# Optimization experiments

Hardware: AMD Instinct MI355X
Metric: run time of the kernel (lower is better)

The kernel has to match this reference:

```python
import jax, jax.numpy as jnp
import numpy as np
from jax import lax

D, B, C, H, HD, FF, NC = 6, 32, 384, 6, 64, 1536, 10
IMG, P = 224, 16
N = (IMG // P) ** 2 + 1  # 197 tokens incl cls
SCALE = HD ** -0.5
EPS = 1e-6


def ln(x, w, b):
    m = jnp.mean(x, axis=-1, keepdims=True)
    v = jnp.var(x, axis=-1, keepdims=True)
    return (x - m) * lax.rsqrt(v + EPS) * w + b


def setup_inputs() -> dict:
    key = jax.random.key(0)
    ks = iter(jax.random.split(key, 40))
    rn = lambda shape, s=0.02: jax.random.normal(next(ks), shape, jnp.float32) * s
    inp = {
        'x': jax.random.normal(next(ks), (B, 3, IMG, IMG), jnp.float32),
        'y': jax.random.randint(next(ks), (B,), 0, NC),
        'patch_w': rn((C, 3, P, P)),
        'patch_b': rn((C,)),
        'cls_token': rn((1, 1, C)),
        'pos_embed': rn((1, N, C)),
        'n1_w': jnp.ones((D, C)), 'n1_b': jnp.zeros((D, C)),
        'qkv_w': rn((D, 3 * C, C)), 'qkv_b': rn((D, 3 * C)),
        'proj_w': rn((D, C, C)), 'proj_b': rn((D, C)),
        'mask_attn': jnp.ones((D, NC, H, HD)) + rn((D, NC, H, HD), 0.01),
        'mask_proj': jnp.ones((D, NC, C, C)) + rn((D, NC, C, C), 0.01),
        'n2_w': jnp.ones((D, C)), 'n2_b': jnp.zeros((D, C)),
        'fc1_w': rn((D, FF, C)), 'fc1_b': rn((D, FF)),
        'fc2_w': rn((D, C, FF)), 'fc2_b': rn((D, C)),
        'mask_fc1': jnp.ones((D, NC, FF, C)) + rn((D, NC, FF, C), 0.01),
        'mask_fc2': jnp.ones((D, NC, C, FF)) + rn((D, NC, C, FF), 0.01),
        'norm_w': jnp.ones((C,)), 'norm_b': jnp.zeros((C,)),
        'head_w': rn((NC, C)), 'head_b': jnp.zeros((NC,)),
    }
    return inp


def reference(x, y, patch_w, patch_b, cls_token, pos_embed, n1_w, n1_b, qkv_w,
              qkv_b, proj_w, proj_b, mask_attn, mask_proj, n2_w, n2_b,
              fc1_w, fc1_b, fc2_w, fc2_b, mask_fc1, mask_fc2,
              norm_w, norm_b, head_w, head_b):
    # patch embed: conv P x P stride P -> (B, C, 14, 14) -> (B, 196, C)
    h = lax.conv_general_dilated(x, patch_w, (P, P), 'VALID',
                                 dimension_numbers=('NCHW', 'OIHW', 'NCHW'))
    h = h.reshape(B, C, -1).transpose(0, 2, 1) + patch_b
    h = jnp.concatenate([jnp.broadcast_to(cls_token, (B, 1, C)), h], axis=1)
    h = h + pos_embed

    def block(xc, p):
        (w1n, b1n, qw, qb, pw, pb, ma, mp, w2n, b2n,
         f1w, f1b, f2w, f2b, mf1, mf2) = p
        t = ln(xc, w1n, b1n)
        qkv = (t @ qw.T + qb).reshape(B, N, 3, H, HD).transpose(2, 0, 3, 1, 4)
        q, k, v = qkv[0], qkv[1], qkv[2]  # (B,H,N,HD)
        a = jax.nn.softmax((q * SCALE) @ k.transpose(0, 1, 3, 2), axis=-1)
        o = a @ v  # (B,H,N,HD)
        o = o * ma[y][:, :, None, :]  # per-class head/dim mask
        o = o.transpose(0, 2, 1, 3).reshape(B, N, C)
        Wp = pw[None] * mp[y]  # (B,C,C) per-sample masked proj
        attn_out = jnp.einsum('bni,boi->bno', o, Wp) + pb
        xc = xc + attn_out
        t = ln(xc, w2n, b2n)
        W1 = f1w[None] * mf1[y]  # (B,FF,C)
        t = jnp.einsum('bni,boi->bno', t, W1) + f1b
        t = jax.nn.gelu(t, approximate=False)
        W2 = f2w[None] * mf2[y]  # (B,C,FF)
        t = jnp.einsum('bni,boi->bno', t, W2) + f2b
        return xc + t, None

    xs = (n1_w, n1_b, qkv_w, qkv_b, proj_w, proj_b, mask_attn, mask_proj,
          n2_w, n2_b, fc1_w, fc1_b, fc2_w, fc2_b, mask_fc1, mask_fc2)
    h, _ = lax.scan(block, h, xs)
    h = ln(h, norm_w, norm_b)
    cls = h[:, 0]  # (B, C)
    return cls @ head_w.T + head_b
```

## Files before the change

### kernel.cpp

```cpp
#include <hip/hip_runtime.h>
#include <hip/hip_bf16.h>
#include <math.h>

#define Dn 6
#define Bn 32
#define Cn 384
#define Hn 6
#define HDn 64
#define FFn 1536
#define NCn 10
#define IMGn 224
#define Nn 197
#define NPATCH 196
#define RP 256
#define SCALEf 0.125f
#define EPSf 1e-6f

typedef unsigned short u16;
typedef __attribute__((ext_vector_type(8))) short short8;
typedef __attribute__((ext_vector_type(4))) float f32x4;

__device__ __forceinline__ u16 f2bf(float f) {
    unsigned u = __float_as_uint(f);
    return (u16)((u + 0x7FFFu + ((u >> 16) & 1u)) >> 16);
}

__device__ __forceinline__ void gload16(const void* g, void* l) {
    __builtin_amdgcn_global_load_lds((const __attribute__((address_space(1))) void*)g,
                                     (__attribute__((address_space(3))) void*)l, 16, 0, 0);
}

__global__ __launch_bounds__(256) void cvtbf_kernel(const float* __restrict__ in,
                                                    u16* __restrict__ out) {
    long off = ((long)blockIdx.x * 256 + threadIdx.x) * 8;
    float4 v0 = *(const float4*)(in + off);
    float4 v1 = *(const float4*)(in + off + 4);
    short8 p;
    p[0] = f2bf(v0.x); p[1] = f2bf(v0.y); p[2] = f2bf(v0.z); p[3] = f2bf(v0.w);
    p[4] = f2bf(v1.x); p[5] = f2bf(v1.y); p[6] = f2bf(v1.z); p[7] = f2bf(v1.w);
    *(short8*)(out + off) = p;
}

__global__ __launch_bounds__(256) void maskmul3_kernel(
    const float* __restrict__ pw, const float* __restrict__ mp,
    const float* __restrict__ f1w, const float* __restrict__ mf1,
    const float* __restrict__ f2w, const float* __restrict__ mf2,
    u16* __restrict__ WMp, u16* __restrict__ WMf1, u16* __restrict__ WMf2) {
    int seg = blockIdx.y;
    const float* W; const float* M; u16* O; int NK; int nblk;
    if (seg == 0)      { W = pw;  M = mp;  O = WMp;  NK = Cn * Cn;  nblk = 720; }
    else if (seg == 1) { W = f1w; M = mf1; O = WMf1; NK = FFn * Cn; nblk = 2880; }
    else               { W = f2w; M = mf2; O = WMf2; NK = Cn * FFn; nblk = 2880; }
    if (blockIdx.x >= nblk) return;
    long e = ((long)blockIdx.x * 256 + threadIdx.x) * 8;
    int c = (int)(e / NK);
    int wi = (int)(e - (long)c * NK);
    float4 w0 = *(const float4*)(W + wi);
    float4 w1 = *(const float4*)(W + wi + 4);
    float4 m0 = *(const float4*)(M + e);
    float4 m1 = *(const float4*)(M + e + 4);
    short8 p;
    p[0] = f2bf(w0.x * m0.x); p[1] = f2bf(w0.y * m0.y);
    p[2] = f2bf(w0.z * m0.z); p[3] = f2bf(w0.w * m0.w);
    p[4] = f2bf(w1.x * m1.x); p[5] = f2bf(w1.y * m1.y);
    p[6] = f2bf(w1.z * m1.z); p[7] = f2bf(w1.w * m1.w);
    *(short8*)(O + e) = p;
}

__global__ __launch_bounds__(256) void im2col_kernel(const float* __restrict__ x,
                                                     u16* __restrict__ col) {
    long idx = (long)blockIdx.x * 256 + threadIdx.x;
    int k = (int)(idx % 768);
    long row = idx / 768;
    int b = (int)(row / NPATCH), p = (int)(row % NPATCH);
    int i = k / 256, r = k % 256, ph = r / 16, pw = r % 16;
    int py = p / 14, px = p % 14;
    col[idx] = f2bf(x[(((long)b * 3 + i) * IMGn + py * 16 + ph) * IMGn + px * 16 + pw]);
}

__global__ __launch_bounds__(256) void assemble_kernel(const float* __restrict__ tmp,
                                                       const float* __restrict__ cls_token,
                                                       const float* __restrict__ pos,
                                                       float* __restrict__ x) {
    long idx = (long)blockIdx.x * 256 + threadIdx.x;
    const long total = (long)Bn * Nn * Cn;
    if (idx >= total) return;
    int c = (int)(idx % Cn);
    long rem = idx / Cn;
    int n = (int)(rem % Nn);
    int b = (int)(rem / Nn);
    float v;
    if (n == 0) v = cls_token[c];
    else v = tmp[((long)b * NPATCH + (n - 1)) * Cn + c];
    x[((long)b * RP + n) * Cn + c] = v + pos[n * Cn + c];
}

__global__ __launch_bounds__(64) void ln_kernel(const float* __restrict__ x,
                                                const float* __restrict__ w,
                                                const float* __restrict__ b,
                                                u16* __restrict__ out) {
    long blk = blockIdx.x;
    int bb = (int)(blk / Nn), n = (int)(blk % Nn);
    long row = (long)bb * RP + n;
    int lane = threadIdx.x;
    const float* xr = x + row * Cn;
    float v[6];
    float s = 0.f, ss = 0.f;
#pragma unroll
    for (int j = 0; j < 6; ++j) {
        v[j] = xr[lane + 64 * j];
        s += v[j];
        ss += v[j] * v[j];
    }
#pragma unroll
    for (int off = 32; off >= 1; off >>= 1) {
        s += __shfl_xor(s, off);
        ss += __shfl_xor(ss, off);
    }
    float m = s * (1.0f / Cn);
    float var = ss * (1.0f / Cn) - m * m;
    float rstd = rsqrtf(var + EPSf);
#pragma unroll
    for (int j = 0; j < 6; ++j) {
        int c = lane + 64 * j;
        out[row * Cn + c] = f2bf((v[j] - m) * rstd * w[c] + b[c]);
    }
}

template <int EPI, int MT>
__global__ __launch_bounds__(256) void gemm_bf16(
    const u16* __restrict__ A, long strideA,
    const u16* __restrict__ Wb, long wClassStride,
    const int* __restrict__ y,
    const float* __restrict__ bias,
    void* __restrict__ OutV, long strideO,
    int Nout, int Ktot) {
    const int bz = blockIdx.z;
    A += (long)bz * strideA;
    const u16* Wp = Wb + (y ? (long)y[bz] * wClassStride : 0);

    constexpr int ASUB = MT / 16;
    constexpr int AI = MT / 32;
    __shared__ alignas(16) u16 Ab[2][ASUB * 512];
    __shared__ alignas(16) u16 Bb[2][4096];

    const int tid = threadIdx.x;
    const int lane = tid & 63;
    const int w = tid >> 6;
    const int wr = w >> 1, wc = w & 1;
    const int m0 = blockIdx.x * MT;
    const int n0 = blockIdx.y * 128;
    const int r15 = lane & 15, oct = lane >> 4;

    auto STAGE = [&](int k0, int bf) {
        {
            int s0 = 2 * w;
            const u16* b0 = Wp + (long)(n0 + 16 * s0 + r15) * Ktot + k0 + oct * 8;
            gload16(b0, &Bb[bf][s0 * 512]);
            gload16(b0 + 16 * (long)Ktot, &Bb[bf][(s0 + 1) * 512]);
        }
        if (MT == 128) {
            int s0 = 2 * w;
            const u16* a0 = A + (long)(m0 + 16 * s0 + r15) * Ktot + k0 + oct * 8;
            gload16(a0, &Ab[bf][s0 * 512]);
            gload16(a0 + 16 * (long)Ktot, &Ab[bf][(s0 + 1) * 512]);
        } else {
            const u16* a0 = A + (long)(m0 + 16 * w + r15) * Ktot + k0 + oct * 8;
            gload16(a0, &Ab[bf][w * 512]);
        }
    };

    f32x4 acc[AI][4];
#pragma unroll
    for (int i = 0; i < AI; ++i)
#pragma unroll
        for (int j = 0; j < 4; ++j) acc[i][j] = (f32x4){0.f, 0.f, 0.f, 0.f};

    const int nsteps = Ktot / 32;
    STAGE(0, 0);
    __syncthreads();
    int cur = 0;
    for (int t = 0; t < nsteps; ++t) {
        if (t + 1 < nsteps) STAGE((t + 1) * 32, cur ^ 1);
        short8 af[AI], bfr[4];
#pragma unroll
        for (int i = 0; i < AI; ++i)
            af[i] = *(const short8*)(&Ab[cur][(wr * AI + i) * 512 + lane * 8]);
#pragma unroll
        for (int j = 0; j < 4; ++j)
            bfr[j] = *(const short8*)(&Bb[cur][(wc * 4 + j) * 512 + lane * 8]);
#pragma unroll
        for (int i = 0; i < AI; ++i)
#pragma unroll
            for (int j = 0; j < 4; ++j)
                acc[i][j] = __builtin_amdgcn_mfma_f32_16x16x32_bf16(af[i], bfr[j], acc[i][j], 0, 0, 0);
        __syncthreads();
        cur ^= 1;
    }

    const int lr = lane >> 4;
    const int lc = lane & 15;
#pragma unroll
    for (int i = 0; i < AI; ++i) {
#pragma unroll
        for (int j = 0; j < 4; ++j) {
            int colg = n0 + (wc * 4 + j) * 16 + lc;
            float bv = bias ? bias[colg] : 0.f;
#pragma unroll
            for (int r = 0; r < 4; ++r) {
                int m = m0 + (wr * AI + i) * 16 + lr * 4 + r;
                float v = acc[i][j][r] + bv;
                long oi = (long)m * Nout + colg;
                if (EPI == 0) {
                    ((u16*)OutV + (long)bz * strideO)[oi] = f2bf(v);
                } else if (EPI == 1) {
                    v = 0.5f * v * (1.0f + erff(v * 0.70710678118654752440f));
                    ((u16*)OutV + (long)bz * strideO)[oi] = f2bf(v);
                } else if (EPI == 2) {
                    float* Out = (float*)OutV + (long)bz * strideO;
                    Out[oi] += v;
                } else {
                    ((float*)OutV + (long)bz * strideO)[oi] = v;
                }
            }
        }
    }
}

__global__ __launch_bounds__(256) void attn_fused(const u16* __restrict__ qkv,
                                                  const float* __restrict__ ma,
                                                  const int* __restrict__ y,
                                                  u16* __restrict__ O) {
    const int it = blockIdx.x;
    const int bh = blockIdx.y;
    const int h = bh % Hn, b = bh / Hn;
    const int i0 = it * 64;
    const int tid = threadIdx.x, lane = tid & 63, w = tid >> 6;
    const int lg = lane >> 4, lc = lane & 15;

    __shared__ alignas(16) u16 SH[31744];
    u16* Qb = SH;
    u16* Kb = SH + 4096;
    u16* Vb = SH;
    u16* Pb = SH + 17408;

    const u16* qkv_b = qkv + (long)b * RP * (3 * Cn);
    const int r15 = lane & 15;
    const int oct = lane >> 4;

#pragma unroll
    for (int si = 0; si < 2; ++si) {
        int s = w * 2 + si;
        int r = (s >> 1) * 16 + r15;
        int g = (s & 1) * 4 + oct;
        const u16* src = qkv_b + (long)(i0 + r) * (3 * Cn) + h * HDn + g * 8;
        gload16(src, Qb + s * 512);
    }
    for (int s = w; s < 26; s += 4) {
        int c = (s >> 1) * 16 + r15;
        int g = (s & 1) * 4 + oct;
        const u16* src = qkv_b + (long)c * (3 * Cn) + Cn + h * HDn + g * 8;
        gload16(src, Kb + s * 512);
    }
    __syncthreads();

    f32x4 s[13];
#pragma unroll
    for (int jf = 0; jf < 13; ++jf) s[jf] = (f32x4){0.f, 0.f, 0.f, 0.f};
    {
        short8 a0 = *(const short8*)(Qb + (w * 2 + 0) * 512 + lane * 8);
        short8 a1 = *(const short8*)(Qb + (w * 2 + 1) * 512 + lane * 8);
#pragma unroll
        for (int jf = 0; jf < 13; ++jf) {
            short8 b0 = *(const short8*)(Kb + (jf * 2 + 0) * 512 + lane * 8);
            short8 b1 = *(const short8*)(Kb + (jf * 2 + 1) * 512 + lane * 8);
            s[jf] = __builtin_amdgcn_mfma_f32_16x16x32_bf16(a0, b0, s[jf], 0, 0, 0);
            s[jf] = __builtin_amdgcn_mfma_f32_16x16x32_bf16(a1, b1, s[jf], 0, 0, 0);
        }
    }

#pragma unroll
    for (int r = 0; r < 4; ++r) {
        float mx = -1e30f;
#pragma unroll
        for (int jf = 0; jf < 13; ++jf) {
            float v = s[jf][r] * SCALEf;
            if (jf * 16 + lc > 196) v = -1e30f;
            mx = fmaxf(mx, v);
        }
#pragma unroll
        for (int off = 1; off <= 8; off <<= 1) mx = fmaxf(mx, __shfl_xor(mx, off));
        float sum = 0.f;
#pragma unroll
        for (int jf = 0; jf < 13; ++jf) {
            float e = (jf * 16 + lc <= 196) ? __expf(s[jf][r] * SCALEf - mx) : 0.f;
            s[jf][r] = e;
            sum += e;
        }
#pragma unroll
        for (int off = 1; off <= 8; off <<= 1) sum += __shfl_xor(sum, off);
        float inv = 1.0f / sum;
#pragma unroll
        for (int jf = 0; jf < 13; ++jf) s[jf][r] *= inv;
    }
    __syncthreads();

    if (lane < 32) {
        short8 z = {0, 0, 0, 0, 0, 0, 0, 0};
        *(short8*)(Pb + (w * 7 + 6) * 512 + (32 + lane) * 8) = z;
    }
#pragma unroll
    for (int jf = 0; jf < 13; ++jf) {
#pragma unroll
        for (int r = 0; r < 4; ++r) {
            int col = jf * 16 + lc;
            int row = lg * 4 + r;
            Pb[(w * 7 + (col >> 5)) * 512 + (((col >> 3) & 3) * 16 + row) * 8 + (col & 7)] =
                (u16)f2bf(s[jf][r]);
        }
    }
    {
        const u16* vbase = qkv_b + 2 * Cn + h * HDn + (tid & 63);
        int d = tid & 63;
#pragma unroll
        for (int k = 0; k < 7; ++k) {
            int jo = (tid >> 6) + 4 * k;
            short8 p;
#pragma unroll
            for (int t = 0; t < 8; ++t)
                p[t] = (short)vbase[(long)(jo * 8 + t) * (3 * Cn)];
            *(short8*)(Vb + (d >> 4) * (7 * 512) + (jo >> 2) * 512 +
                       ((jo & 3) * 16 + (d & 15)) * 8) = p;
        }
    }
    __syncthreads();

    f32x4 o[4];
#pragma unroll
    for (int df = 0; df < 4; ++df) o[df] = (f32x4){0.f, 0.f, 0.f, 0.f};
#pragma unroll
    for (int ks = 0; ks < 7; ++ks) {
        short8 pa = *(const short8*)(Pb + (w * 7 + ks) * 512 + lane * 8);
#pragma unroll
        for (int df = 0; df < 4; ++df) {
            short8 vb = *(const short8*)(Vb + (df * 7 + ks) * 512 + lane * 8);
            o[df] = __builtin_amdgcn_mfma_f32_16x16x32_bf16(pa, vb, o[df], 0, 0, 0);
        }
    }

    const float* mar = ma + (long)y[b] * (Hn * HDn) + h * HDn;
#pragma unroll
    for (int df = 0; df < 4; ++df) {
        int dcol = df * 16 + lc;
        float mk = mar[dcol];
#pragma unroll
        for (int r = 0; r < 4; ++r) {
            int i = i0 + w * 16 + lg * 4 + r;
            O[((long)b * RP + i) * Cn + h * HDn + dcol] = f2bf(o[df][r] * mk);
        }
    }
}

__global__ __launch_bounds__(64) void final_head(const float* __restrict__ x,
                                                 const float* __restrict__ nw,
                                                 const float* __restrict__ nb,
                                                 const float* __restrict__ hw,
                                                 const float* __restrict__ hb,
                                                 float* __restrict__ out) {
    int b = blockIdx.x;
    int lane = threadIdx.x;
    const float* xr = x + (long)b * RP * Cn;
    float v[6];
    float s = 0.f, ss = 0.f;
#pragma unroll
    for (int j = 0; j < 6; ++j) {
        v[j] = xr[lane + 64 * j];
        s += v[j];
        ss += v[j] * v[j];
    }
#pragma unroll
    for (int off = 32; off >= 1; off >>= 1) {
        s += __shfl_xor(s, off);
        ss += __shfl_xor(ss, off);
    }
    float m = s * (1.0f / Cn);
    float var = ss * (1.0f / Cn) - m * m;
    float rstd = rsqrtf(var + EPSf);
    float nvals[6];
#pragma unroll
    for (int j = 0; j < 6; ++j) {
        int c = lane + 64 * j;
        nvals[j] = (v[j] - m) * rstd * nw[c] + nb[c];
    }
    for (int c10 = 0; c10 < NCn; ++c10) {
        float p = 0.f;
#pragma unroll
        for (int j = 0; j < 6; ++j) p += nvals[j] * hw[(long)c10 * Cn + lane + 64 * j];
#pragma unroll
        for (int off = 32; off >= 1; off >>= 1) p += __shfl_xor(p, off);
        if (lane == 0) out[b * NCn + c10] = p + hb[c10];
    }
}

extern "C" void kernel_launch(void* const* d_in, const int* in_sizes, int n_in,
                              void* d_out, int out_size, void* d_ws, size_t ws_size,
                              hipStream_t stream) {
    const float* x_in     = (const float*)d_in[0];
    const int*   y        = (const int*)d_in[1];
    const float* patch_w  = (const float*)d_in[2];
    const float* patch_b  = (const float*)d_in[3];
    const float* cls_tok  = (const float*)d_in[4];
    const float* pos_emb  = (const float*)d_in[5];
    const float* n1_w     = (const float*)d_in[6];
    const float* n1_b     = (const float*)d_in[7];
    const float* qkv_w    = (const float*)d_in[8];
    const float* qkv_b    = (const float*)d_in[9];
    const float* proj_w   = (const float*)d_in[10];
    const float* proj_b   = (const float*)d_in[11];
    const float* mask_attn= (const float*)d_in[12];
    const float* mask_proj= (const float*)d_in[13];
    const float* n2_w     = (const float*)d_in[14];
    const float* n2_b     = (const float*)d_in[15];
    const float* fc1_w    = (const float*)d_in[16];
    const float* fc1_b    = (const float*)d_in[17];
    const float* fc2_w    = (const float*)d_in[18];
    const float* fc2_b    = (const float*)d_in[19];
    const float* mask_fc1 = (const float*)d_in[20];
    const float* mask_fc2 = (const float*)d_in[21];
    const float* norm_w   = (const float*)d_in[22];
    const float* norm_b   = (const float*)d_in[23];
    const float* head_w   = (const float*)d_in[24];
    const float* head_b   = (const float*)d_in[25];

    char* base = (char*)d_ws;
    float* X   = (float*)base;                       base += (long)Bn * RP * Cn * 4;
    u16*   T   = (u16*)base;                         base += (long)Bn * RP * Cn * 2;
    u16*   QKV = (u16*)base;                         base += (long)Bn * RP * 3 * Cn * 2;
    u16*   O   = (u16*)base;                         base += (long)Bn * RP * Cn * 2;
    u16*   FFb = (u16*)base;                         base += (long)Bn * RP * FFn * 2;
    u16*   COL = (u16*)base;                         base += (long)Bn * NPATCH * 768 * 2;
    u16*   WQ  = (u16*)base;                         base += (long)Dn * 3 * Cn * Cn * 2;
    u16*   WP  = (u16*)base;                         base += (long)Cn * 768 * 2;
    u16*   WMp = (u16*)base;                         base += (long)NCn * Cn * Cn * 2;
    u16*   WMf1= (u16*)base;                         base += (long)NCn * FFn * Cn * 2;
    u16*   WMf2= (u16*)base;                         base += (long)NCn * Cn * FFn * 2;
    float* PTMP= (float*)FFb;

    const long sX = (long)RP * Cn;
    const long sT = (long)RP * Cn;
    const long sF = (long)RP * FFn;

    cvtbf_kernel<<<1296, 256, 0, stream>>>(qkv_w, WQ);
    cvtbf_kernel<<<144, 256, 0, stream>>>(patch_w, WP);

    im2col_kernel<<<18816, 256, 0, stream>>>(x_in, COL);
    gemm_bf16<3, 64><<<dim3(98, 3, 1), 256, 0, stream>>>(
        COL, 0, WP, 0, nullptr, patch_b, PTMP, 0, Cn, 768);
    assemble_kernel<<<9456, 256, 0, stream>>>(PTMP, cls_tok, pos_emb, X);

    for (int l = 0; l < Dn; ++l) {
        maskmul3_kernel<<<dim3(2880, 3), 256, 0, stream>>>(
            proj_w + (long)l * Cn * Cn, mask_proj + (long)l * NCn * Cn * Cn,
            fc1_w + (long)l * FFn * Cn, mask_fc1 + (long)l * NCn * FFn * Cn,
            fc2_w + (long)l * Cn * FFn, mask_fc2 + (long)l * NCn * Cn * FFn,
            WMp, WMf1, WMf2);

        ln_kernel<<<Bn * Nn, 64, 0, stream>>>(X, n1_w + l * Cn, n1_b + l * Cn, T);
        gemm_bf16<0, 128><<<dim3(64, 9, 1), 256, 0, stream>>>(
            T, 0, WQ + (long)l * 3 * Cn * Cn, 0, nullptr, qkv_b + (long)l * 3 * Cn,
            QKV, 0, 3 * Cn, Cn);
        attn_fused<<<dim3(4, Bn * Hn), 256, 0, stream>>>(
            QKV, mask_attn + (long)l * NCn * Hn * HDn, y, O);
        gemm_bf16<2, 64><<<dim3(4, 3, Bn), 256, 0, stream>>>(
            O, sT, WMp, (long)Cn * Cn, y, proj_b + l * Cn, X, sX, Cn, Cn);
        ln_kernel<<<Bn * Nn, 64, 0, stream>>>(X, n2_w + l * Cn, n2_b + l * Cn, T);
        gemm_bf16<1, 128><<<dim3(2, 12, Bn), 256, 0, stream>>>(
            T, sT, WMf1, (long)FFn * Cn, y, fc1_b + (long)l * FFn, FFb, sF, FFn, Cn);
        gemm_bf16<2, 64><<<dim3(4, 3, Bn), 256, 0, stream>>>(
            FFb, sF, WMf2, (long)Cn * FFn, y, fc2_b + l * Cn, X, sX, Cn, FFn);
    }

    final_head<<<Bn, 64, 0, stream>>>(X, norm_w, norm_b, head_w, head_b, (float*)d_out);
}
```

Baseline: 1.023 ms.

## Fuse residual add and LayerNorm into full-row GEMM epilogues, batch mask prep

Adds a gemm_ln kernel that computes full 384-wide output rows per block, so the residual add and the following LayerNorm run in the GEMM epilogue. This removes the standalone ln_kernel launches and the extra passes over X. The patch-embed GEMM also folds in the pos-embed add and the first LN, and a small kernel handles the cls token and zeroes the pad rows. Mask-weight products for all layers are now built in one up-front launch instead of once per layer, at the cost of more workspace. The proj and fc2 GEMMs now launch only 4 row-tiles per sample (128 blocks) with 24 accumulators per wave, which may reduce occupancy and parallelism.

```diff
diff --git a/kernel.cpp b/kernel.cpp
--- a/kernel.cpp
+++ b/kernel.cpp
@@ -41,16 +41,24 @@
     *(short8*)(out + off) = p;
 }
 
-__global__ __launch_bounds__(256) void maskmul3_kernel(
+__global__ __launch_bounds__(256) void maskmul_all(
     const float* __restrict__ pw, const float* __restrict__ mp,
     const float* __restrict__ f1w, const float* __restrict__ mf1,
     const float* __restrict__ f2w, const float* __restrict__ mf2,
     u16* __restrict__ WMp, u16* __restrict__ WMf1, u16* __restrict__ WMf2) {
+    int l = blockIdx.z;
     int seg = blockIdx.y;
     const float* W; const float* M; u16* O; int NK; int nblk;
-    if (seg == 0)      { W = pw;  M = mp;  O = WMp;  NK = Cn * Cn;  nblk = 720; }
-    else if (seg == 1) { W = f1w; M = mf1; O = WMf1; NK = FFn * Cn; nblk = 2880; }
-    else               { W = f2w; M = mf2; O = WMf2; NK = Cn * FFn; nblk = 2880; }
+    if (seg == 0) {
+        W = pw + (long)l * Cn * Cn; M = mp + (long)l * NCn * Cn * Cn;
+        O = WMp + (long)l * NCn * Cn * Cn; NK = Cn * Cn; nblk = 720;
+    } else if (seg == 1) {
+        W = f1w + (long)l * FFn * Cn; M = mf1 + (long)l * NCn * FFn * Cn;
+        O = WMf1 + (long)l * NCn * FFn * Cn; NK = FFn * Cn; nblk = 2880;
+    } else {
+        W = f2w + (long)l * Cn * FFn; M = mf2 + (long)l * NCn * Cn * FFn;
+        O = WMf2 + (long)l * NCn * Cn * FFn; NK = Cn * FFn; nblk = 2880;
+    }
     if (blockIdx.x >= nblk) return;
     long e = ((long)blockIdx.x * 256 + threadIdx.x) * 8;
     int c = (int)(e / NK);
@@ -78,101 +86,85 @@
     col[idx] = f2bf(x[(((long)b * 3 + i) * IMGn + py * 16 + ph) * IMGn + px * 16 + pw]);
 }
 
-__global__ __launch_bounds__(256) void assemble_kernel(const float* __restrict__ tmp,
-                                                       const float* __restrict__ cls_token,
-                                                       const float* __restrict__ pos,
-                                                       float* __restrict__ x) {
-    long idx = (long)blockIdx.x * 256 + threadIdx.x;
-    const long total = (long)Bn * Nn * Cn;
-    if (idx >= total) return;
-    int c = (int)(idx % Cn);
-    long rem = idx / Cn;
-    int n = (int)(rem % Nn);
-    int b = (int)(rem / Nn);
-    float v;
-    if (n == 0) v = cls_token[c];
-    else v = tmp[((long)b * NPATCH + (n - 1)) * Cn + c];
-    x[((long)b * RP + n) * Cn + c] = v + pos[n * Cn + c];
-}
-
-__global__ __launch_bounds__(64) void ln_kernel(const float* __restrict__ x,
-                                                const float* __restrict__ w,
-                                                const float* __restrict__ b,
-                                                u16* __restrict__ out) {
-    long blk = blockIdx.x;
-    int bb = (int)(blk / Nn), n = (int)(blk % Nn);
-    long row = (long)bb * RP + n;
-    int lane = threadIdx.x;
-    const float* xr = x + row * Cn;
-    float v[6];
-    float s = 0.f, ss = 0.f;
-#pragma unroll
-    for (int j = 0; j < 6; ++j) {
-        v[j] = xr[lane + 64 * j];
-        s += v[j];
-        ss += v[j] * v[j];
-    }
-#pragma unroll
-    for (int off = 32; off >= 1; off >>= 1) {
-        s += __shfl_xor(s, off);
-        ss += __shfl_xor(ss, off);
-    }
-    float m = s * (1.0f / Cn);
-    float var = ss * (1.0f / Cn) - m * m;
-    float rstd = rsqrtf(var + EPSf);
-#pragma unroll
-    for (int j = 0; j < 6; ++j) {
-        int c = lane + 64 * j;
-        out[row * Cn + c] = f2bf((v[j] - m) * rstd * w[c] + b[c]);
-    }
-}
-
-template <int EPI, int MT>
+__global__ __launch_bounds__(256) void clspad_kernel(const float* __restrict__ cls,
+                                                     const float* __restrict__ pos,
+                                                     const float* __restrict__ nw,
+                                                     const float* __restrict__ nb,
+                                                     float* __restrict__ X,
+                                                     u16* __restrict__ T) {
+    int b = blockIdx.x;
+    int tid = threadIdx.x;
+    float* Xb = X + (long)b * RP * Cn;
+    u16* Tb = T + (long)b * RP * Cn;
+    if (tid < 64) {
+        float v[6];
+        float s = 0.f, ss = 0.f;
+#pragma unroll
+        for (int j = 0; j < 6; ++j) {
+            int c = tid + 64 * j;
+            v[j] = cls[c] + pos[c];
+            s += v[j]; ss += v[j] * v[j];
+        }
+#pragma unroll
+        for (int off = 32; off >= 1; off >>= 1) {
+            s += __shfl_xor(s, off);
+            ss += __shfl_xor(ss, off);
+        }
+        float m = s * (1.0f / Cn);
+        float rstd = rsqrtf(ss * (1.0f / Cn) - m * m + EPSf);
+#pragma unroll
+        for (int j = 0; j < 6; ++j) {
+            int c = tid + 64 * j;
+            Xb[c] = v[j];
+            Tb[c] = f2bf((v[j] - m) * rstd * nw[c] + nb[c]);
+        }
+    } else {
+        int t = tid - 64;
+        for (int idx = t; idx < 59 * Cn; idx += 192) {
+            int row = 197 + idx / Cn, col = idx % Cn;
+            Xb[(long)row * Cn + col] = 0.f;
+            Tb[(long)row * Cn + col] = 0;
+        }
+    }
+}
+
+template <int EPI>
 __global__ __launch_bounds__(256) void gemm_bf16(
     const u16* __restrict__ A, long strideA,
     const u16* __restrict__ Wb, long wClassStride,
     const int* __restrict__ y,
     const float* __restrict__ bias,
-    void* __restrict__ OutV, long strideO,
+    u16* __restrict__ Out, long strideO,
     int Nout, int Ktot) {
     const int bz = blockIdx.z;
     A += (long)bz * strideA;
     const u16* Wp = Wb + (y ? (long)y[bz] * wClassStride : 0);
-
-    constexpr int ASUB = MT / 16;
-    constexpr int AI = MT / 32;
-    __shared__ alignas(16) u16 Ab[2][ASUB * 512];
+    Out += (long)bz * strideO;
+
+    __shared__ alignas(16) u16 Ab[2][4096];
     __shared__ alignas(16) u16 Bb[2][4096];
 
     const int tid = threadIdx.x;
     const int lane = tid & 63;
     const int w = tid >> 6;
     const int wr = w >> 1, wc = w & 1;
-    const int m0 = blockIdx.x * MT;
+    const int m0 = blockIdx.x * 128;
     const int n0 = blockIdx.y * 128;
     const int r15 = lane & 15, oct = lane >> 4;
 
     auto STAGE = [&](int k0, int bf) {
-        {
-            int s0 = 2 * w;
-            const u16* b0 = Wp + (long)(n0 + 16 * s0 + r15) * Ktot + k0 + oct * 8;
-            gload16(b0, &Bb[bf][s0 * 512]);
-            gload16(b0 + 16 * (long)Ktot, &Bb[bf][(s0 + 1) * 512]);
-        }
-        if (MT == 128) {
-            int s0 = 2 * w;
-            const u16* a0 = A + (long)(m0 + 16 * s0 + r15) * Ktot + k0 + oct * 8;
-            gload16(a0, &Ab[bf][s0 * 512]);
-            gload16(a0 + 16 * (long)Ktot, &Ab[bf][(s0 + 1) * 512]);
-        } else {
-            const u16* a0 = A + (long)(m0 + 16 * w + r15) * Ktot + k0 + oct * 8;
-            gload16(a0, &Ab[bf][w * 512]);
-        }
+        int s0 = 2 * w;
+        const u16* b0 = Wp + (long)(n0 + 16 * s0 + r15) * Ktot + k0 + oct * 8;
+        gload16(b0, &Bb[bf][s0 * 512]);
+        gload16(b0 + 16 * (long)Ktot, &Bb[bf][(s0 + 1) * 512]);
+        const u16* a0 = A + (long)(m0 + 16 * s0 + r15) * Ktot + k0 + oct * 8;
+        gload16(a0, &Ab[bf][s0 * 512]);
+        gload16(a0 + 16 * (long)Ktot, &Ab[bf][(s0 + 1) * 512]);
     };
 
-    f32x4 acc[AI][4];
-#pragma unroll
-    for (int i = 0; i < AI; ++i)
+    f32x4 acc[4][4];
+#pragma unroll
+    for (int i = 0; i < 4; ++i)
 #pragma unroll
         for (int j = 0; j < 4; ++j) acc[i][j] = (f32x4){0.f, 0.f, 0.f, 0.f};
 
@@ -182,15 +174,15 @@
     int cur = 0;
     for (int t = 0; t < nsteps; ++t) {
         if (t + 1 < nsteps) STAGE((t + 1) * 32, cur ^ 1);
-        short8 af[AI], bfr[4];
-#pragma unroll
-        for (int i = 0; i < AI; ++i)
-            af[i] = *(const short8*)(&Ab[cur][(wr * AI + i) * 512 + lane * 8]);
+        short8 af[4], bfr[4];
+#pragma unroll
+        for (int i = 0; i < 4; ++i)
+            af[i] = *(const short8*)(&Ab[cur][(wr * 4 + i) * 512 + lane * 8]);
 #pragma unroll
         for (int j = 0; j < 4; ++j)
             bfr[j] = *(const short8*)(&Bb[cur][(wc * 4 + j) * 512 + lane * 8]);
 #pragma unroll
-        for (int i = 0; i < AI; ++i)
+        for (int i = 0; i < 4; ++i)
 #pragma unroll
             for (int j = 0; j < 4; ++j)
                 acc[i][j] = __builtin_amdgcn_mfma_f32_16x16x32_bf16(af[i], bfr[j], acc[i][j], 0, 0, 0);
@@ -201,28 +193,111 @@
     const int lr = lane >> 4;
     const int lc = lane & 15;
 #pragma unroll
-    for (int i = 0; i < AI; ++i) {
+    for (int i = 0; i < 4; ++i) {
 #pragma unroll
         for (int j = 0; j < 4; ++j) {
             int colg = n0 + (wc * 4 + j) * 16 + lc;
             float bv = bias ? bias[colg] : 0.f;
 #pragma unroll
             for (int r = 0; r < 4; ++r) {
-                int m = m0 + (wr * AI + i) * 16 + lr * 4 + r;
+                int m = m0 + (wr * 4 + i) * 16 + lr * 4 + r;
                 float v = acc[i][j][r] + bv;
-                long oi = (long)m * Nout + colg;
-                if (EPI == 0) {
-                    ((u16*)OutV + (long)bz * strideO)[oi] = f2bf(v);
-                } else if (EPI == 1) {
-                    v = 0.5f * v * (1.0f + erff(v * 0.70710678118654752440f));
-                    ((u16*)OutV + (long)bz * strideO)[oi] = f2bf(v);
-                } else if (EPI == 2) {
-                    float* Out = (float*)OutV + (long)bz * strideO;
-                    Out[oi] += v;
-                } else {
-                    ((float*)OutV + (long)bz * strideO)[oi] = v;
-                }
+                if (EPI == 1) v = 0.5f * v * (1.0f + erff(v * 0.70710678118654752440f));
+                Out[(long)m * Nout + colg] = f2bf(v);
             }
+        }
+    }
+}
+
+template <int MODE>
+__global__ __launch_bounds__(256) void gemm_ln(
+    const u16* __restrict__ A, long strideA,
+    const u16* __restrict__ Wb, long wcs,
+    const int* __restrict__ y,
+    const float* __restrict__ bias,
+    float* __restrict__ X, u16* __restrict__ T,
+    const float* __restrict__ pos,
+    const float* __restrict__ nw, const float* __restrict__ nb,
+    int Ktot) {
+    const int bz = (MODE == 1) ? blockIdx.y : 0;
+    const u16* Ap = A + (long)bz * strideA;
+    const u16* Wp = Wb + ((MODE == 1 && y) ? (long)y[bz] * wcs : 0);
+    float* Xb = X + ((MODE == 1) ? (long)bz * RP * Cn : 0);
+    u16* Tb = T + ((MODE == 1) ? (long)bz * RP * Cn : 0);
+
+    __shared__ alignas(16) u16 Ab[2][2048];
+    __shared__ alignas(16) u16 Bb[2][12288];
+
+    const int tid = threadIdx.x, lane = tid & 63, w = tid >> 6;
+    const int m0 = blockIdx.x * 64;
+    const int r15 = lane & 15, oct = lane >> 4;
+
+    auto STAGE = [&](int k0, int bf) {
+        gload16(Ap + (long)(m0 + 16 * w + r15) * Ktot + k0 + oct * 8, &Ab[bf][w * 512]);
+#pragma unroll
+        for (int i = 0; i < 6; ++i) {
+            int s = w * 6 + i;
+            gload16(Wp + (long)(16 * s + r15) * Ktot + k0 + oct * 8, &Bb[bf][s * 512]);
+        }
+    };
+
+    f32x4 acc[24];
+#pragma unroll
+    for (int j = 0; j < 24; ++j) acc[j] = (f32x4){0.f, 0.f, 0.f, 0.f};
+
+    const int nsteps = Ktot / 32;
+    STAGE(0, 0);
+    __syncthreads();
+    int cur = 0;
+    for (int t = 0; t < nsteps; ++t) {
+        if (t + 1 < nsteps) STAGE((t + 1) * 32, cur ^ 1);
+        short8 af = *(const short8*)(&Ab[cur][w * 512 + lane * 8]);
+#pragma unroll
+        for (int j = 0; j < 24; ++j) {
+            short8 bf16f = *(const short8*)(&Bb[cur][j * 512 + lane * 8]);
+            acc[j] = __builtin_amdgcn_mfma_f32_16x16x32_bf16(af, bf16f, acc[j], 0, 0, 0);
+        }
+        __syncthreads();
+        cur ^= 1;
+    }
+
+    const int lg = lane >> 4, lc = lane & 15;
+#pragma unroll
+    for (int r = 0; r < 4; ++r) {
+        int row_l = w * 16 + lg * 4 + r;
+        long xrow;
+        const float* posr = nullptr;
+        if (MODE == 0) {
+            int pr = m0 + row_l;
+            int b = pr / NPATCH, p = pr - b * NPATCH;
+            xrow = (long)b * RP + 1 + p;
+            posr = pos + (long)(1 + p) * Cn;
+        } else {
+            xrow = m0 + row_l;
+        }
+        float s = 0.f, ss = 0.f;
+#pragma unroll
+        for (int j = 0; j < 24; ++j) {
+            int col = j * 16 + lc;
+            float v = acc[j][r] + bias[col];
+            if (MODE == 0) v += posr[col];
+            else v += Xb[xrow * Cn + col];
+            acc[j][r] = v;
+            s += v; ss += v * v;
+        }
+#pragma unroll
+        for (int off = 1; off <= 8; off <<= 1) {
+            s += __shfl_xor(s, off);
+            ss += __shfl_xor(ss, off);
+        }
+        float m = s * (1.0f / Cn);
+        float rstd = rsqrtf(ss * (1.0f / Cn) - m * m + EPSf);
+#pragma unroll
+        for (int j = 0; j < 24; ++j) {
+            int col = j * 16 + lc;
+            float v = acc[j][r];
+            Xb[xrow * Cn + col] = v;
+            Tb[xrow * Cn + col] = f2bf((v - m) * rstd * nw[col] + nb[col]);
         }
     }
 }
@@ -433,51 +508,51 @@
     const float* head_b   = (const float*)d_in[25];
 
     char* base = (char*)d_ws;
-    float* X   = (float*)base;                       base += (long)Bn * RP * Cn * 4;
-    u16*   T   = (u16*)base;                         base += (long)Bn * RP * Cn * 2;
-    u16*   QKV = (u16*)base;                         base += (long)Bn * RP * 3 * Cn * 2;
-    u16*   O   = (u16*)base;                         base += (long)Bn * RP * Cn * 2;
-    u16*   FFb = (u16*)base;                         base += (long)Bn * RP * FFn * 2;
-    u16*   COL = (u16*)base;                         base += (long)Bn * NPATCH * 768 * 2;
-    u16*   WQ  = (u16*)base;                         base += (long)Dn * 3 * Cn * Cn * 2;
-    u16*   WP  = (u16*)base;                         base += (long)Cn * 768 * 2;
-    u16*   WMp = (u16*)base;                         base += (long)NCn * Cn * Cn * 2;
-    u16*   WMf1= (u16*)base;                         base += (long)NCn * FFn * Cn * 2;
-    u16*   WMf2= (u16*)base;                         base += (long)NCn * Cn * FFn * 2;
-    float* PTMP= (float*)FFb;
-
-    const long sX = (long)RP * Cn;
+    float* X    = (float*)base;   base += (long)Bn * RP * Cn * 4;
+    u16*   T    = (u16*)base;     base += (long)Bn * RP * Cn * 2;
+    u16*   QKV  = (u16*)base;     base += (long)Bn * RP * 3 * Cn * 2;
+    u16*   O    = (u16*)base;     base += (long)Bn * RP * Cn * 2;
+    u16*   FFb  = (u16*)base;     base += (long)Bn * RP * FFn * 2;
+    u16*   COL  = (u16*)base;     base += (long)Bn * NPATCH * 768 * 2;
+    u16*   WQ   = (u16*)base;     base += (long)Dn * 3 * Cn * Cn * 2;
+    u16*   WP   = (u16*)base;     base += (long)Cn * 768 * 2;
+    u16*   WMp  = (u16*)base;     base += (long)Dn * NCn * Cn * Cn * 2;
+    u16*   WMf1 = (u16*)base;     base += (long)Dn * NCn * FFn * Cn * 2;
+    u16*   WMf2 = (u16*)base;     base += (long)Dn * NCn * Cn * FFn * 2;
+
     const long sT = (long)RP * Cn;
     const long sF = (long)RP * FFn;
 
     cvtbf_kernel<<<1296, 256, 0, stream>>>(qkv_w, WQ);
     cvtbf_kernel<<<144, 256, 0, stream>>>(patch_w, WP);
+    maskmul_all<<<dim3(2880, 3, Dn), 256, 0, stream>>>(
+        proj_w, mask_proj, fc1_w, mask_fc1, fc2_w, mask_fc2, WMp, WMf1, WMf2);
 
     im2col_kernel<<<18816, 256, 0, stream>>>(x_in, COL);
-    gemm_bf16<3, 64><<<dim3(98, 3, 1), 256, 0, stream>>>(
-        COL, 0, WP, 0, nullptr, patch_b, PTMP, 0, Cn, 768);
-    assemble_kernel<<<9456, 256, 0, stream>>>(PTMP, cls_tok, pos_emb, X);
+    clspad_kernel<<<Bn, 256, 0, stream>>>(cls_tok, pos_emb, n1_w, n1_b, X, T);
+    gemm_ln<0><<<dim3(98), 256, 0, stream>>>(
+        COL, 0, WP, 0, nullptr, patch_b, X, T, pos_emb, n1_w, n1_b, 768);
 
     for (int l = 0; l < Dn; ++l) {
-        maskmul3_kernel<<<dim3(2880, 3), 256, 0, stream>>>(
-            proj_w + (long)l * Cn * Cn, mask_proj + (long)l * NCn * Cn * Cn,
-            fc1_w + (long)l * FFn * Cn, mask_fc1 + (long)l * NCn * FFn * Cn,
-            fc2_w + (long)l * Cn * FFn, mask_fc2 + (long)l * NCn * Cn * FFn,
-            WMp, WMf1, WMf2);
-
-        ln_kernel<<<Bn * Nn, 64, 0, stream>>>(X, n1_w + l * Cn, n1_b + l * Cn, T);
-        gemm_bf16<0, 128><<<dim3(64, 9, 1), 256, 0, stream>>>(
+        const u16* WMp_l  = WMp  + (long)l * NCn * Cn * Cn;
+        const u16* WMf1_l = WMf1 + (long)l * NCn * FFn * Cn;
+        const u16* WMf2_l = WMf2 + (long)l * NCn * Cn * FFn;
+        const float* n1n = n1_w + ((l + 1) % Dn) * Cn;
+        const float* n1nb = n1_b + ((l + 1) % Dn) * Cn;
+
+        gemm_bf16<0><<<dim3(64, 9, 1), 256, 0, stream>>>(
             T, 0, WQ + (long)l * 3 * Cn * Cn, 0, nullptr, qkv_b + (long)l * 3 * Cn,
             QKV, 0, 3 * Cn, Cn);
         attn_fused<<<dim3(4, Bn * Hn), 256, 0, stream>>>(
             QKV, mask_attn + (long)l * NCn * Hn * HDn, y, O);
-        gemm_bf16<2, 64><<<dim3(4, 3, Bn), 256, 0, stream>>>(
-            O, sT, WMp, (long)Cn * Cn, y, proj_b + l * Cn, X, sX, Cn, Cn);
-        ln_kernel<<<Bn * Nn, 64, 0, stream>>>(X, n2_w + l * Cn, n2_b + l * Cn, T);
-        gemm_bf16<1, 128><<<dim3(2, 12, Bn), 256, 0, stream>>>(
-            T, sT, WMf1, (long)FFn * Cn, y, fc1_b + (long)l * FFn, FFb, sF, FFn, Cn);
-        gemm_bf16<2, 64><<<dim3(4, 3, Bn), 256, 0, stream>>>(
-            FFb, sF, WMf2, (long)Cn * FFn, y, fc2_b + l * Cn, X, sX, Cn, FFn);
+        gemm_ln<1><<<dim3(4, Bn), 256, 0, stream>>>(
+            O, sT, WMp_l, (long)Cn * Cn, y, proj_b + l * Cn,
+            X, T, nullptr, n2_w + l * Cn, n2_b + l * Cn, Cn);
+        gemm_bf16<1><<<dim3(2, 12, Bn), 256, 0, stream>>>(
+            T, sT, WMf1_l, (long)FFn * Cn, y, fc1_b + (long)l * FFn, FFb, sF, FFn, Cn);
+        gemm_ln<1><<<dim3(4, Bn), 256, 0, stream>>>(
+            FFb, sF, WMf2_l, (long)Cn * FFn, y, fc2_b + l * Cn,
+            X, T, nullptr, n1n, n1nb, FFn);
     }
 
     final_head<<<Bn, 64, 0, stream>>>(X, norm_w, norm_b, head_w, head_b, (float*)d_out);
```

After: 1.389 ms. 1.36x slower.

## Pack token rows for QKV GEMM and hoist mask-weight products out of layer loop

Applied to the files above, without the earlier changes.

Moves the per-layer masked-weight bf16 conversion into one up-front launch over all layers, with wider per-thread work and nontemporal loads of the masks. LayerNorm output now uses a packed layout with 197 rows per sample (6400 rows total, zero-padded), so the QKV GEMM covers only real tokens using 64-row tiles. This removes padded-row work from the QKV GEMM and cuts the per-layer launch count. The cost is six times more workspace for the masked weights, and the fc1 GEMM now reads A tiles that straddle sample boundaries, which relies on correct padding handling.

```diff
diff --git a/kernel.cpp b/kernel.cpp
--- a/kernel.cpp
+++ b/kernel.cpp
@@ -13,6 +13,7 @@
 #define Nn 197
 #define NPATCH 196
 #define RP 256
+#define TROWS 6400
 #define SCALEf 0.125f
 #define EPSf 1e-6f
 
@@ -41,30 +42,50 @@
     *(short8*)(out + off) = p;
 }
 
-__global__ __launch_bounds__(256) void maskmul3_kernel(
+__global__ __launch_bounds__(256) void maskmul_all(
     const float* __restrict__ pw, const float* __restrict__ mp,
     const float* __restrict__ f1w, const float* __restrict__ mf1,
     const float* __restrict__ f2w, const float* __restrict__ mf2,
     u16* __restrict__ WMp, u16* __restrict__ WMf1, u16* __restrict__ WMf2) {
-    int seg = blockIdx.y;
-    const float* W; const float* M; u16* O; int NK; int nblk;
-    if (seg == 0)      { W = pw;  M = mp;  O = WMp;  NK = Cn * Cn;  nblk = 720; }
-    else if (seg == 1) { W = f1w; M = mf1; O = WMf1; NK = FFn * Cn; nblk = 2880; }
-    else               { W = f2w; M = mf2; O = WMf2; NK = Cn * FFn; nblk = 2880; }
-    if (blockIdx.x >= nblk) return;
-    long e = ((long)blockIdx.x * 256 + threadIdx.x) * 8;
-    int c = (int)(e / NK);
-    int wi = (int)(e - (long)c * NK);
-    float4 w0 = *(const float4*)(W + wi);
-    float4 w1 = *(const float4*)(W + wi + 4);
-    float4 m0 = *(const float4*)(M + e);
-    float4 m1 = *(const float4*)(M + e + 4);
-    short8 p;
-    p[0] = f2bf(w0.x * m0.x); p[1] = f2bf(w0.y * m0.y);
-    p[2] = f2bf(w0.z * m0.z); p[3] = f2bf(w0.w * m0.w);
-    p[4] = f2bf(w1.x * m1.x); p[5] = f2bf(w1.y * m1.y);
-    p[6] = f2bf(w1.z * m1.z); p[7] = f2bf(w1.w * m1.w);
-    *(short8*)(O + e) = p;
+    const int l = blockIdx.z;
+    const int seg = blockIdx.y;
+    const unsigned bx = blockIdx.x;
+    const float* W; const float* M; u16* O; long e;
+    if (seg == 0) {
+        if (bx >= 360u) return;
+        unsigned cls = bx / 36u;
+        e = (long)(bx - cls * 36u) * 4096 + threadIdx.x * 16;
+        W = pw + (long)l * (Cn * Cn);
+        M = mp + ((long)l * NCn + cls) * (Cn * Cn) + e;
+        O = WMp + ((long)l * NCn + cls) * (Cn * Cn) + e;
+    } else if (seg == 1) {
+        unsigned cls = bx / 144u;
+        e = (long)(bx - cls * 144u) * 4096 + threadIdx.x * 16;
+        W = f1w + (long)l * (FFn * Cn);
+        M = mf1 + ((long)l * NCn + cls) * (FFn * Cn) + e;
+        O = WMf1 + ((long)l * NCn + cls) * (FFn * Cn) + e;
+    } else {
+        unsigned cls = bx / 144u;
+        e = (long)(bx - cls * 144u) * 4096 + threadIdx.x * 16;
+        W = f2w + (long)l * (Cn * FFn);
+        M = mf2 + ((long)l * NCn + cls) * (Cn * FFn) + e;
+        O = WMf2 + ((long)l * NCn + cls) * (Cn * FFn) + e;
+    }
+    const f32x4* w4 = (const f32x4*)(W + e);
+    const f32x4* m4 = (const f32x4*)M;
+#pragma unroll
+    for (int h = 0; h < 2; ++h) {
+        f32x4 w0 = w4[2 * h];
+        f32x4 w1 = w4[2 * h + 1];
+        f32x4 m0 = __builtin_nontemporal_load(m4 + 2 * h);
+        f32x4 m1 = __builtin_nontemporal_load(m4 + 2 * h + 1);
+        short8 p;
+        p[0] = f2bf(w0[0] * m0[0]); p[1] = f2bf(w0[1] * m0[1]);
+        p[2] = f2bf(w0[2] * m0[2]); p[3] = f2bf(w0[3] * m0[3]);
+        p[4] = f2bf(w1[0] * m1[0]); p[5] = f2bf(w1[1] * m1[1]);
+        p[6] = f2bf(w1[2] * m1[2]); p[7] = f2bf(w1[3] * m1[3]);
+        *(short8*)(O + 8 * h) = p;
+    }
 }
 
 __global__ __launch_bounds__(256) void im2col_kernel(const float* __restrict__ x,
@@ -83,8 +104,6 @@
                                                        const float* __restrict__ pos,
                                                        float* __restrict__ x) {
     long idx = (long)blockIdx.x * 256 + threadIdx.x;
-    const long total = (long)Bn * Nn * Cn;
-    if (idx >= total) return;
     int c = (int)(idx % Cn);
     long rem = idx / Cn;
     int n = (int)(rem % Nn);
@@ -95,15 +114,28 @@
     x[((long)b * RP + n) * Cn + c] = v + pos[n * Cn + c];
 }
 
+__global__ __launch_bounds__(256) void pad_zero(float* __restrict__ X,
+                                                u16* __restrict__ Tp) {
+    int b = blockIdx.x;
+    int tid = threadIdx.x;
+    if (b == Bn) {
+        u16* t0 = Tp + (long)Bn * Nn * Cn;
+        for (int i = tid; i < (TROWS - Bn * Nn) * Cn; i += 256) t0[i] = 0;
+        return;
+    }
+    float* Xb = X + ((long)b * RP + Nn) * Cn;
+    for (int i = tid; i < (RP - Nn) * Cn; i += 256) Xb[i] = 0.f;
+}
+
 __global__ __launch_bounds__(64) void ln_kernel(const float* __restrict__ x,
                                                 const float* __restrict__ w,
                                                 const float* __restrict__ b,
                                                 u16* __restrict__ out) {
     long blk = blockIdx.x;
     int bb = (int)(blk / Nn), n = (int)(blk % Nn);
-    long row = (long)bb * RP + n;
+    const float* xr = x + ((long)bb * RP + n) * Cn;
+    u16* orow = out + ((long)bb * Nn + n) * Cn;
     int lane = threadIdx.x;
-    const float* xr = x + row * Cn;
     float v[6];
     float s = 0.f, ss = 0.f;
 #pragma unroll
@@ -123,7 +155,7 @@
 #pragma unroll
     for (int j = 0; j < 6; ++j) {
         int c = lane + 64 * j;
-        out[row * Cn + c] = f2bf((v[j] - m) * rstd * w[c] + b[c]);
+        orow[c] = f2bf((v[j] - m) * rstd * w[c] + b[c]);
     }
 }
 
@@ -217,8 +249,7 @@
                     v = 0.5f * v * (1.0f + erff(v * 0.70710678118654752440f));
                     ((u16*)OutV + (long)bz * strideO)[oi] = f2bf(v);
                 } else if (EPI == 2) {
-                    float* Out = (float*)OutV + (long)bz * strideO;
-                    Out[oi] += v;
+                    ((float*)OutV + (long)bz * strideO)[oi] += v;
                 } else {
                     ((float*)OutV + (long)bz * strideO)[oi] = v;
                 }
@@ -244,7 +275,7 @@
     u16* Vb = SH;
     u16* Pb = SH + 17408;
 
-    const u16* qkv_b = qkv + (long)b * RP * (3 * Cn);
+    const u16* qkv_b = qkv + (long)b * Nn * (3 * Cn);
     const int r15 = lane & 15;
     const int oct = lane >> 4;
 
@@ -433,51 +464,54 @@
     const float* head_b   = (const float*)d_in[25];
 
     char* base = (char*)d_ws;
-    float* X   = (float*)base;                       base += (long)Bn * RP * Cn * 4;
-    u16*   T   = (u16*)base;                         base += (long)Bn * RP * Cn * 2;
-    u16*   QKV = (u16*)base;                         base += (long)Bn * RP * 3 * Cn * 2;
-    u16*   O   = (u16*)base;                         base += (long)Bn * RP * Cn * 2;
-    u16*   FFb = (u16*)base;                         base += (long)Bn * RP * FFn * 2;
-    u16*   COL = (u16*)base;                         base += (long)Bn * NPATCH * 768 * 2;
-    u16*   WQ  = (u16*)base;                         base += (long)Dn * 3 * Cn * Cn * 2;
-    u16*   WP  = (u16*)base;                         base += (long)Cn * 768 * 2;
-    u16*   WMp = (u16*)base;                         base += (long)NCn * Cn * Cn * 2;
-    u16*   WMf1= (u16*)base;                         base += (long)NCn * FFn * Cn * 2;
-    u16*   WMf2= (u16*)base;                         base += (long)NCn * Cn * FFn * 2;
-    float* PTMP= (float*)FFb;
+    float* X    = (float*)base;   base += (long)Bn * RP * Cn * 4;
+    u16*   Tp   = (u16*)base;     base += (long)TROWS * Cn * 2;
+    u16*   QKV  = (u16*)base;     base += (long)TROWS * 3 * Cn * 2;
+    u16*   O    = (u16*)base;     base += (long)Bn * RP * Cn * 2;
+    u16*   FFb  = (u16*)base;     base += (long)Bn * RP * FFn * 2;
+    u16*   COL  = (u16*)base;     base += (long)Bn * NPATCH * 768 * 2;
+    u16*   WQ   = (u16*)base;     base += (long)Dn * 3 * Cn * Cn * 2;
+    u16*   WP   = (u16*)base;     base += (long)Cn * 768 * 2;
+    u16*   WMp  = (u16*)base;     base += (long)Dn * NCn * Cn * Cn * 2;
+    u16*   WMf1 = (u16*)base;     base += (long)Dn * NCn * FFn * Cn * 2;
+    u16*   WMf2 = (u16*)base;     base += (long)Dn * NCn * Cn * FFn * 2;
+    float* PTMP = (float*)FFb;
 
     const long sX = (long)RP * Cn;
-    const long sT = (long)RP * Cn;
+    const long sTp = (long)Nn * Cn;
     const long sF = (long)RP * FFn;
 
     cvtbf_kernel<<<1296, 256, 0, stream>>>(qkv_w, WQ);
     cvtbf_kernel<<<144, 256, 0, stream>>>(patch_w, WP);
+    maskmul_all<<<dim3(1440, 3, Dn), 256, 0, stream>>>(
+        proj_w, mask_proj, fc1_w, mask_fc1, fc2_w, mask_fc2, WMp, WMf1, WMf2);
 
     im2col_kernel<<<18816, 256, 0, stream>>>(x_in, COL);
     gemm_bf16<3, 64><<<dim3(98, 3, 1), 256, 0, stream>>>(
         COL, 0, WP, 0, nullptr, patch_b, PTMP, 0, Cn, 768);
     assemble_kernel<<<9456, 256, 0, stream>>>(PTMP, cls_tok, pos_emb, X);
+    pad_zero<<<Bn + 1, 256, 0, stream>>>(X, Tp);
+    ln_kernel<<<Bn * Nn, 64, 0, stream>>>(X, n1_w, n1_b, Tp);
 
     for (int l = 0; l < Dn; ++l) {
-        maskmul3_kernel<<<dim3(2880, 3), 256, 0, stream>>>(
-            proj_w + (long)l * Cn * Cn, mask_proj + (long)l * NCn * Cn * Cn,
-            fc1_w + (long)l * FFn * Cn, mask_fc1 + (long)l * NCn * FFn * Cn,
-            fc2_w + (long)l * Cn * FFn, mask_fc2 + (long)l * NCn * Cn * FFn,
-            WMp, WMf1, WMf2);
-
-        ln_kernel<<<Bn * Nn, 64, 0, stream>>>(X, n1_w + l * Cn, n1_b + l * Cn, T);
-        gemm_bf16<0, 128><<<dim3(64, 9, 1), 256, 0, stream>>>(
-            T, 0, WQ + (long)l * 3 * Cn * Cn, 0, nullptr, qkv_b + (long)l * 3 * Cn,
+        const u16* WMp_l  = WMp  + (long)l * NCn * Cn * Cn;
+        const u16* WMf1_l = WMf1 + (long)l * NCn * FFn * Cn;
+        const u16* WMf2_l = WMf2 + (long)l * NCn * Cn * FFn;
+
+        gemm_bf16<0, 64><<<dim3(100, 9, 1), 256, 0, stream>>>(
+            Tp, 0, WQ + (long)l * 3 * Cn * Cn, 0, nullptr, qkv_b + (long)l * 3 * Cn,
             QKV, 0, 3 * Cn, Cn);
         attn_fused<<<dim3(4, Bn * Hn), 256, 0, stream>>>(
             QKV, mask_attn + (long)l * NCn * Hn * HDn, y, O);
         gemm_bf16<2, 64><<<dim3(4, 3, Bn), 256, 0, stream>>>(
-            O, sT, WMp, (long)Cn * Cn, y, proj_b + l * Cn, X, sX, Cn, Cn);
-        ln_kernel<<<Bn * Nn, 64, 0, stream>>>(X, n2_w + l * Cn, n2_b + l * Cn, T);
+            O, sX, WMp_l, (long)Cn * Cn, y, proj_b + l * Cn, X, sX, Cn, Cn);
+        ln_kernel<<<Bn * Nn, 64, 0, stream>>>(X, n2_w + l * Cn, n2_b + l * Cn, Tp);
         gemm_bf16<1, 128><<<dim3(2, 12, Bn), 256, 0, stream>>>(
-            T, sT, WMf1, (long)FFn * Cn, y, fc1_b + (long)l * FFn, FFb, sF, FFn, Cn);
+            Tp, sTp, WMf1_l, (long)FFn * Cn, y, fc1_b + (long)l * FFn, FFb, sF, FFn, Cn);
         gemm_bf16<2, 64><<<dim3(4, 3, Bn), 256, 0, stream>>>(
-            FFb, sF, WMf2, (long)Cn * FFn, y, fc2_b + l * Cn, X, sX, Cn, FFn);
+            FFb, sF, WMf2_l, (long)Cn * FFn, y, fc2_b + l * Cn, X, sX, Cn, FFn);
+        if (l + 1 < Dn)
+            ln_kernel<<<Bn * Nn, 64, 0, stream>>>(X, n1_w + (l + 1) * Cn, n1_b + (l + 1) * Cn, Tp);
     }
 
     final_head<<<Bn, 64, 0, stream>>>(X, norm_w, norm_b, head_w, head_b, (float*)d_out);
```

New measurement: 1.075 ms. +5.1%, slower.
